# Optimization experiments

Measured on AMD Instinct MI355X. Metric: run time of the kernel, lower is better.

Reference implementation:

```python
import jax, jax.numpy as jnp
from jax import lax
import numpy as np

B, N, D_IN = 8, 8192, 16
GROUP_NUM, K = 512, 32
OUT_DIM, N_BLOCKS, DIM_EXP = 256, 2, 2
PREV_DIM = OUT_DIM // DIM_EXP   # 128
MID = OUT_DIM // 2              # bottleneck width in FeatureTransform
C_EXP = 2 * PREV_DIM + 3        # linear1 input channels
EPS = 1e-5                      # BatchNorm eps (eval mode, running stats mean=0 var=1)


def setup_inputs() -> dict:
    ks = jax.random.split(jax.random.key(0), 8)
    return {
        "xyz": jax.random.normal(ks[0], (B, N, 3), jnp.float32),
        "feat": jax.random.normal(ks[1], (B, N, D_IN), jnp.float32),
        "w_embed": jax.random.normal(ks[2], (PREV_DIM, D_IN), jnp.float32) * 0.1,
        "b_embed": jnp.zeros((PREV_DIM,), jnp.float32),
        "g_embed": jnp.ones((PREV_DIM,), jnp.float32),
        "be_embed": jnp.zeros((PREV_DIM,), jnp.float32),
        "w_lin1": jax.random.normal(ks[3], (OUT_DIM, C_EXP), jnp.float32) * 0.05,
        "g_lin1": jnp.ones((OUT_DIM,), jnp.float32),
        "be_lin1": jnp.zeros((OUT_DIM,), jnp.float32),
        "down_w": jax.random.normal(ks[4], (N_BLOCKS, MID, OUT_DIM), jnp.float32) * 0.05,
        "down_b": jnp.zeros((N_BLOCKS, MID), jnp.float32),
        "gd": jnp.ones((N_BLOCKS, MID), jnp.float32),
        "bd": jnp.zeros((N_BLOCKS, MID), jnp.float32),
        "up_w": jax.random.normal(ks[5], (N_BLOCKS, OUT_DIM, MID), jnp.float32) * 0.05,
        "up_b": jnp.zeros((N_BLOCKS, OUT_DIM), jnp.float32),
        "gu": jnp.ones((N_BLOCKS, OUT_DIM), jnp.float32),
        "bu": jnp.zeros((N_BLOCKS, OUT_DIM), jnp.float32),
    }


def _bn(x, g, b, axis):
    # eval-mode BatchNorm with running mean=0, var=1
    shp = [1] * x.ndim
    shp[axis] = -1
    return x / jnp.sqrt(1.0 + EPS) * g.reshape(shp) + b.reshape(shp)


def _fps(xyz, n):
    # deterministic FPS (eval mode): start from point farthest from origin
    Bb, Nn, _ = xyz.shape
    cur0 = jnp.argmax(jnp.sum(xyz * xyz, -1), axis=1)          # [B]
    mind0 = jnp.full((Bb, Nn), 1e10, xyz.dtype)

    def step(carry, _):
        cur, mind = carry
        c = jnp.take_along_axis(xyz, cur[:, None, None], axis=1)  # [B,1,3]
        mind = jnp.minimum(mind, jnp.sum((xyz - c) ** 2, -1))
        return (jnp.argmax(mind, axis=1), mind), cur

    _, sel = lax.scan(step, (cur0, mind0), None, length=n)     # sel: [n,B]
    return sel.T                                               # [B,n]


def _gather(points, idx):
    # points [B,N,C], idx [B,...] -> [B,...,C]
    Bb = points.shape[0]
    flat = idx.reshape(Bb, -1)
    out = jnp.take_along_axis(points, flat[:, :, None], axis=1)
    return out.reshape(idx.shape + (points.shape[-1],))


def _knn(k, ref, query):
    # squared dists, clamped at 0 as in pairwise_sq_dist
    d = (jnp.sum(query * query, -1)[:, :, None]
         + jnp.sum(ref * ref, -1)[:, None, :]
         - 2.0 * jnp.einsum('bsc,bnc->bsn', query, ref))
    d = jnp.maximum(d, 0.0)
    _, idx = lax.top_k(-d, k)
    return idx  # [B,S,k]


def reference(xyz, feat, w_embed, b_embed, g_embed, be_embed, w_lin1, g_lin1, be_lin1,
              down_w, down_b, gd, bd, up_w, up_b, gu, bu):
    # PointEmbed: conv1d(1x1) + BN + ReLU on per-point features -> [B,N,PREV_DIM]
    f0 = jnp.einsum('bnc,dc->bnd', feat, w_embed) + b_embed
    f0 = jax.nn.relu(_bn(f0, g_embed, be_embed, axis=2))

    # FpsKnnGroup
    sel = _fps(xyz, GROUP_NUM)                  # [B,G]
    lc_xyz = _gather(xyz, sel)                  # [B,G,3]
    lc_feat = _gather(f0, sel)                  # [B,G,PREV_DIM]
    nn_idx = _knn(K, xyz, lc_xyz)               # [B,G,K]
    knn_xyz = _gather(xyz, nn_idx)              # [B,G,K,3]
    knn_feat = jnp.concatenate([_gather(f0, nn_idx), knn_xyz], axis=-1)  # [B,G,K,PREV+3]

    # LocalGeoAgg, norm_type='mn40'
    anchor = lc_xyz[:, :, None, :]
    rel_raw = knn_xyz - anchor
    std = jnp.std(rel_raw, ddof=1) + 1e-5       # torch .std() is unbiased
    knn_xyz_n = rel_raw / std
    Bc = knn_feat.shape[0]
    expanded = jnp.concatenate(
        [knn_feat, jnp.broadcast_to(lc_feat[:, :, None, :], (Bc, GROUP_NUM, K, PREV_DIM))],
        axis=-1)                                # [B,G,K,C_EXP]
    x = jnp.einsum('bgkc,dc->bdgk', expanded, w_lin1)   # linear1 (no bias)
    x = jax.nn.relu(_bn(x, g_lin1, be_lin1, axis=1))    # [B,OUT_DIM,G,K]

    # GaussianPosEnc: rel = normalized knn_xyz (perm) minus raw lc_xyz center
    rel = knn_xyz_n.transpose(0, 3, 1, 2) - lc_xyz.transpose(0, 2, 1)[:, :, :, None]
    w = jnp.exp(-jnp.linalg.norm(rel, axis=1) / 2.0)    # sigma=1 -> 2*sigma^2=2
    x = x * w[:, None, :, :]

    # FeatureTransform residual bottlenecks
    for i in range(N_BLOCKS):
        h = jnp.einsum('bcgk,mc->bmgk', x, down_w[i]) + down_b[i][None, :, None, None]
        h = jax.nn.relu(_bn(h, gd[i], bd[i], axis=1))
        h = jnp.einsum('bcgk,mc->bmgk', h, up_w[i]) + up_b[i][None, :, None, None]
        h = _bn(h, gu[i], bu[i], axis=1)
        x = jax.nn.relu(h + x)

    # MaxMeanPool over K
    return jnp.max(x, axis=-1) + jnp.mean(x, axis=-1)   # [B,OUT_DIM,G]
```

## Files before the change

kernel.cpp:

```cpp
#include <hip/hip_runtime.h>

#define B_ 8
#define N_ 8192
#define DIN_ 16
#define G_ 512
#define K_ 32
#define OD_ 256
#define PD_ 128
#define MD_ 128
#define CE_ 259
#define EST 168
#define XST2 264
#define HST 136
#define AL1K 160

typedef __attribute__((ext_vector_type(8))) short short8t;
typedef __attribute__((ext_vector_type(4))) float f32x4;
typedef __attribute__((ext_vector_type(2))) float v2f;
#define MFMA16(a, b, c) __builtin_amdgcn_mfma_f32_16x16x32_bf16((a), (b), (c), 0, 0, 0)

__device__ __forceinline__ ushort bf16_rne(float x) {
    unsigned u = __float_as_uint(x);
    return (ushort)((u + 0x7FFFu + ((u >> 16) & 1u)) >> 16);
}
__device__ __forceinline__ void bf16_split(float x, ushort& h, ushort& l) {
    h = bf16_rne(x);
    float hf = __uint_as_float((unsigned)h << 16);
    l = bf16_rne(x - hf);
}

#define DPP_STEP_MAXF(x, ctrl) { int _t = __builtin_amdgcn_update_dpp(            \
        __float_as_int(x), __float_as_int(x), (ctrl), 0xF, 0xF, false);           \
        (x) = fmaxf((x), __int_as_float(_t)); }
#define DPP_STEP_MINF(x, ctrl) { int _t = __builtin_amdgcn_update_dpp(            \
        __float_as_int(x), __float_as_int(x), (ctrl), 0xF, 0xF, false);           \
        (x) = fminf((x), __int_as_float(_t)); }
#define DPP_STEP_MINU(x, ctrl) { int _t = __builtin_amdgcn_update_dpp(            \
        (int)(x), (int)(x), (ctrl), 0xF, 0xF, false);                             \
        unsigned _u = (unsigned)_t; (x) = ((x) < _u) ? (x) : _u; }

__device__ __forceinline__ float wave_max_f32(float x) {
    DPP_STEP_MAXF(x, 0x121); DPP_STEP_MAXF(x, 0x122);
    DPP_STEP_MAXF(x, 0x124); DPP_STEP_MAXF(x, 0x128);
    DPP_STEP_MAXF(x, 0x142); DPP_STEP_MAXF(x, 0x143);
    return __int_as_float(__builtin_amdgcn_readlane(__float_as_int(x), 63));
}
__device__ __forceinline__ float wave_min_f32(float x) {
    DPP_STEP_MINF(x, 0x121); DPP_STEP_MINF(x, 0x122);
    DPP_STEP_MINF(x, 0x124); DPP_STEP_MINF(x, 0x128);
    DPP_STEP_MINF(x, 0x142); DPP_STEP_MINF(x, 0x143);
    return __int_as_float(__builtin_amdgcn_readlane(__float_as_int(x), 63));
}
__device__ __forceinline__ unsigned wave_min_u32(unsigned x) {
    DPP_STEP_MINU(x, 0x121); DPP_STEP_MINU(x, 0x122);
    DPP_STEP_MINU(x, 0x124); DPP_STEP_MINU(x, 0x128);
    DPP_STEP_MINU(x, 0x142); DPP_STEP_MINU(x, 0x143);
    return (unsigned)__builtin_amdgcn_readlane((int)x, 63);
}

__global__ __launch_bounds__(256)
void prep_kernel(const float* __restrict__ w_lin1, const float* __restrict__ down_w,
                 const float* __restrict__ up_w, const float* __restrict__ w_embed,
                 float* __restrict__ wta, float* __restrict__ wEtg,
                 ushort* __restrict__ alf, ushort* __restrict__ adf,
                 ushort* __restrict__ auf) {
    int i = blockIdx.x * blockDim.x + threadIdx.x;
    if (i < PD_ * OD_) {
        int j = i >> 8, c = i & 255;
        wta[i] = w_lin1[c * CE_ + 131 + j];
    }
    if (i < DIN_ * PD_) {
        int r = i >> 7, c = i & 127;
        wEtg[i] = w_embed[c * DIN_ + r];
    }
    if (i < 5120) {
        int lane = i & 63, t = i >> 6;
        int kbi = t % 5, mtile = t / 5;
        int m = mtile * 16 + (lane & 15), g16 = lane >> 4;
        int dst = i * 8;
#pragma unroll
        for (int j = 0; j < 8; ++j) {
            int k = kbi * 32 + g16 * 8 + j;
            float v = (k < 131) ? w_lin1[m * CE_ + k] : 0.f;
            ushort h, l; bf16_split(v, h, l);
            alf[dst + j] = h; alf[dst + j + 40960] = l;
        }
    }
    if (i < 8192) {
        int lane = i & 63, t = i >> 6;
        int kbi = t & 7, mtile = (t >> 3) & 7, l = t >> 6;
        int m = mtile * 16 + (lane & 15), g16 = lane >> 4;
        int dst = i * 8;
#pragma unroll
        for (int j = 0; j < 8; ++j) {
            int k = kbi * 32 + g16 * 8 + j;
            float v = down_w[(l * MD_ + m) * OD_ + k];
            ushort h, lo; bf16_split(v, h, lo);
            adf[dst + j] = h; adf[dst + j + 65536] = lo;
        }
    }
    if (i < 8192) {
        int lane = i & 63, t = i >> 6;
        int kbi = t & 3, mtile = (t >> 2) & 15, l = t >> 6;
        int m = mtile * 16 + (lane & 15), g16 = lane >> 4;
        int dst = i * 8;
#pragma unroll
        for (int j = 0; j < 8; ++j) {
            int k = kbi * 32 + g16 * 8 + j;
            float v = up_w[(l * OD_ + m) * MD_ + k];
            ushort h, lo; bf16_split(v, h, lo);
            auf[dst + j] = h; auf[dst + j + 65536] = lo;
        }
    }
}

__global__ __launch_bounds__(512)
void fps_kernel(const float* __restrict__ xyz, int* __restrict__ sel) {
#pragma clang fp contract(off)
    __shared__ float sx[N_], sy[N_], sz[N_];
    __shared__ unsigned long long wred[2][8];
    __shared__ int sel_s[G_];
    int b = blockIdx.x, tid = threadIdx.x;
    const float* xb = xyz + (size_t)b * N_ * 3;
    for (int i = tid; i < N_; i += 512) {
        sx[i] = xb[i * 3]; sy[i] = xb[i * 3 + 1]; sz[i] = xb[i * 3 + 2];
    }
    __syncthreads();
    v2f px2[8], py2[8], pz2[8], mind2[8];
    float bv = -1.f; int bj = 0;
#pragma unroll
    for (int p = 0; p < 8; ++p) {
        int i0 = tid + (2 * p) * 512, i1 = tid + (2 * p + 1) * 512;
        px2[p] = (v2f){sx[i0], sx[i1]};
        py2[p] = (v2f){sy[i0], sy[i1]};
        pz2[p] = (v2f){sz[i0], sz[i1]};
        mind2[p] = (v2f){1e10f, 1e10f};
        v2f ss = px2[p] * px2[p] + py2[p] * py2[p];
        ss = ss + pz2[p] * pz2[p];
        if (ss[0] > bv) { bv = ss[0]; bj = 2 * p; }
        if (ss[1] > bv) { bv = ss[1]; bj = 2 * p + 1; }
    }
    int bi = tid + bj * 512;
    int wv = tid >> 6;
    {
        float wm = wave_max_f32(bv);
        unsigned mi = (bv == wm) ? (unsigned)bi : 0xFFFFFFFFu;
        unsigned wi = wave_min_u32(mi);
        if ((tid & 63) == 0)
            wred[0][wv] = ((unsigned long long)__float_as_uint(wm) << 32)
                        | (unsigned long long)(0xFFFFFFFFu - wi);
    }
    __syncthreads();
    unsigned long long best = wred[0][0];
#pragma unroll
    for (int i = 1; i < 8; ++i) { unsigned long long v = wred[0][i]; if (v > best) best = v; }
    int cur = (int)(0xFFFFFFFFu - (unsigned)(best & 0xFFFFFFFFull));

    for (int it = 0; it < G_; ++it) {
        if (tid == 0) sel_s[it] = cur;
        float cx = sx[cur], cy = sy[cur], cz = sz[cur];
        v2f cx2 = (v2f){cx, cx}, cy2 = (v2f){cy, cy}, cz2 = (v2f){cz, cz};
#pragma unroll
        for (int p = 0; p < 8; ++p) {
            v2f dx = px2[p] - cx2, dy = py2[p] - cy2, dz = pz2[p] - cz2;
            v2f d = dx * dx + dy * dy;
            d = d + dz * dz;
            mind2[p] = __builtin_elementwise_min(mind2[p], d);
        }
        bv = -1.f; bj = 0;
#pragma unroll
        for (int j = 0; j < 16; ++j) {
            float m = mind2[j >> 1][j & 1];
            if (m > bv) { bv = m; bj = j; }
        }
        bi = tid + bj * 512;
        float wm = wave_max_f32(bv);
        unsigned mi = (bv == wm) ? (unsigned)bi : 0xFFFFFFFFu;
        unsigned wi = wave_min_u32(mi);
        int pb = (it + 1) & 1;
        if ((tid & 63) == 0)
            wred[pb][wv] = ((unsigned long long)__float_as_uint(wm) << 32)
                         | (unsigned long long)(0xFFFFFFFFu - wi);
        __syncthreads();
        best = wred[pb][0];
#pragma unroll
        for (int i = 1; i < 8; ++i) { unsigned long long v = wred[pb][i]; if (v > best) best = v; }
        cur = (int)(0xFFFFFFFFu - (unsigned)(best & 0xFFFFFFFFull));
    }
    __syncthreads();
    sel[b * G_ + tid] = sel_s[tid];
}

__global__ __launch_bounds__(256)
void knn_kernel(const float* __restrict__ xyz, const int* __restrict__ sel,
                int* __restrict__ nn) {
#pragma clang fp contract(off)
    __shared__ float dld[N_];
    __shared__ unsigned long long wred[2][4];
    __shared__ int nn_s[K_];
    int gb = blockIdx.x; int b = gb >> 9, s = gb & (G_ - 1);
    const float* xb = xyz + (size_t)b * N_ * 3;
    int q = sel[b * G_ + s];
    float qx = xb[q * 3], qy = xb[q * 3 + 1], qz = xb[q * 3 + 2];
    float qq = (qx * qx + qy * qy) + qz * qz;
    int tid = threadIdx.x;
    const float FINF = __builtin_inff();
    float lv = FINF; int li = tid;
#pragma unroll 4
    for (int j = 0; j < 32; ++j) {
        int n = tid + j * 256;
        float rx = xb[n * 3], ry = xb[n * 3 + 1], rz = xb[n * 3 + 2];
        float rr = (rx * rx + ry * ry) + rz * rz;
        float dt = (qx * rx + qy * ry) + qz * rz;
        float d = (qq + rr) - 2.0f * dt;
        d = fmaxf(d, 0.f);
        dld[n] = d;
        if (d < lv) { lv = d; li = n; }
    }
    {
        float wm = wave_min_f32(lv);
        unsigned mi = (lv == wm) ? (unsigned)li : 0xFFFFFFFFu;
        unsigned wi = wave_min_u32(mi);
        if ((tid & 63) == 0)
            wred[0][tid >> 6] = ((unsigned long long)__float_as_uint(wm) << 32)
                              | (unsigned long long)wi;
    }
    __syncthreads();
    unsigned long long best = wred[0][0];
#pragma unroll
    for (int i = 1; i < 4; ++i) { unsigned long long v = wred[0][i]; if (v < best) best = v; }
    int win = (int)(best & 0xFFFFFFFFull);

    for (int t = 0; t < K_; ++t) {
        if (tid == 0) nn_s[t] = win;
        if ((win & 255) == tid) {
            dld[win] = FINF;
            lv = FINF; li = tid;
            for (int j = 0; j < 32; ++j) {
                float d = dld[tid + j * 256];
                if (d < lv) { lv = d; li = tid + j * 256; }
            }
        }
        float wm = wave_min_f32(lv);
        unsigned mi = (lv == wm) ? (unsigned)li : 0xFFFFFFFFu;
        unsigned wi = wave_min_u32(mi);
        int pb = (t + 1) & 1;
        if ((tid & 63) == 0)
            wred[pb][tid >> 6] = ((unsigned long long)__float_as_uint(wm) << 32)
                               | (unsigned long long)wi;
        __syncthreads();
        best = wred[pb][0];
#pragma unroll
        for (int i = 1; i < 4; ++i) { unsigned long long v = wred[pb][i]; if (v < best) best = v; }
        win = (int)(best & 0xFFFFFFFFull);
    }
    if (tid < K_) nn[(size_t)gb * K_ + tid] = nn_s[tid];
}

__global__ void std_acc_kernel(const float* __restrict__ xyz, const int* __restrict__ sel,
                               const int* __restrict__ nn, double* __restrict__ acc) {
    int tot = B_ * G_ * K_;
    int stride = gridDim.x * blockDim.x;
    double ls = 0.0, lss = 0.0;
    for (int idx = blockIdx.x * blockDim.x + threadIdx.x; idx < tot; idx += stride) {
        int b = idx >> 14; int g = (idx >> 5) & (G_ - 1);
        int n = nn[idx]; int a = sel[b * G_ + g];
        const float* xb = xyz + (size_t)b * N_ * 3;
#pragma unroll
        for (int c = 0; c < 3; ++c) {
            float v = xb[n * 3 + c] - xb[a * 3 + c];
            ls += (double)v; lss += (double)v * (double)v;
        }
    }
#pragma unroll
    for (int off = 32; off > 0; off >>= 1) {
        ls += __shfl_down(ls, off); lss += __shfl_down(lss, off);
    }
    if ((threadIdx.x & 63) == 0) { atomicAdd(acc, ls); atomicAdd(acc + 1, lss); }
}

__global__ void std_fin_kernel(const double* __restrict__ acc, float* __restrict__ stdp) {
    double s = acc[0], ss = acc[1];
    double M = (double)(B_ * G_ * K_ * 3);
    double var = (ss - s * s / M) / (M - 1.0);
    stdp[0] = (float)sqrt(var) + 1e-5f;
}

__global__ __launch_bounds__(256, 3)
void group_kernel(const float* __restrict__ xyz, const float* __restrict__ feat,
                  const float* __restrict__ wEtg, const float* __restrict__ bE,
                  const float* __restrict__ gE, const float* __restrict__ beE,
                  const int* __restrict__ sel, const int* __restrict__ nn,
                  const float* __restrict__ wta,
                  const ushort* __restrict__ alf, const ushort* __restrict__ adf,
                  const ushort* __restrict__ auf,
                  const float* __restrict__ g_lin1, const float* __restrict__ be_lin1,
                  const float* __restrict__ down_b, const float* __restrict__ gd,
                  const float* __restrict__ bd,
                  const float* __restrict__ up_b, const float* __restrict__ gu,
                  const float* __restrict__ bu,
                  const float* __restrict__ stdp, float* __restrict__ out) {
    __shared__ __align__(16) ushort smem[25600];
    __shared__ float lcv_s[OD_];
    __shared__ float wk_s[K_];
    __shared__ int nns_s[K_];
    __shared__ float anch[3];
    ushort* XTh = smem;
    ushort* XTl = smem + 8448;
    ushort* HTh = smem + 16896;
    ushort* HTl = smem + 21248;
    ushort* Ehi = XTh;
    ushort* Elo = XTl;
    float* wEt = (float*)(smem + 16896);
    float* fL  = wEt + 2048;
    float* lcf = fL + 544;

    int gb = blockIdx.x; int b = gb >> 9, g = gb & (G_ - 1);
    int tid = threadIdx.x;
    const float* xb = xyz + (size_t)b * N_ * 3;
    int a = sel[b * G_ + g];
    if (tid < K_) nns_s[tid] = nn[(size_t)gb * K_ + tid];
    if (tid < 3)  anch[tid] = xb[a * 3 + tid];
    __syncthreads();

    for (int idx = tid; idx < DIN_ * PD_; idx += 256) wEt[idx] = wEtg[idx];
    const float* fb = feat + (size_t)b * N_ * DIN_;
    for (int idx = tid; idx < 33 * DIN_; idx += 256) {
        int k = idx >> 4, j = idx & 15;
        int n = (k < K_) ? nns_s[k] : a;
        fL[idx] = fb[(size_t)n * DIN_ + j];
    }
    __syncthreads();

    const float s_bn = 1.0f / sqrtf(1.0f + 1e-5f);
    for (int t = tid; t < 33 * 32; t += 256) {
        int k = t >> 5, c0 = (t & 31) * 4;
        const float* f = &fL[k * DIN_];
        float a0 = 0.f, a1 = 0.f, a2 = 0.f, a3 = 0.f;
#pragma unroll
        for (int i = 0; i < DIN_; ++i) {
            float4 w4 = *(const float4*)&wEt[i * PD_ + c0];
            float fv = f[i];
            a0 += w4.x * fv; a1 += w4.y * fv; a2 += w4.z * fv; a3 += w4.w * fv;
        }
        float4 b4  = *(const float4*)&bE[c0];
        float4 g4  = *(const float4*)&gE[c0];
        float4 be4 = *(const float4*)&beE[c0];
        float o0 = fmaxf((a0 + b4.x) * s_bn * g4.x + be4.x, 0.f);
        float o1 = fmaxf((a1 + b4.y) * s_bn * g4.y + be4.y, 0.f);
        float o2 = fmaxf((a2 + b4.z) * s_bn * g4.z + be4.z, 0.f);
        float o3 = fmaxf((a3 + b4.w) * s_bn * g4.w + be4.w, 0.f);
        if (k < K_) {
            ushort h0, l0, h1, l1, h2, l2, h3, l3;
            bf16_split(o0, h0, l0); bf16_split(o1, h1, l1);
            bf16_split(o2, h2, l2); bf16_split(o3, h3, l3);
            *(ushort4*)&Ehi[k * EST + c0] = make_ushort4(h0, h1, h2, h3);
            *(ushort4*)&Elo[k * EST + c0] = make_ushort4(l0, l1, l2, l3);
        } else {
            *(float4*)&lcf[c0] = make_float4(o0, o1, o2, o3);
        }
    }
    for (int idx = tid; idx < K_ * 32; idx += 256) {
        int k = idx >> 5, c = 128 + (idx & 31);
        ushort h = 0, l = 0;
        if (c < 131) { float v = xb[nns_s[k] * 3 + (c - 128)]; bf16_split(v, h, l); }
        Ehi[k * EST + c] = h; Elo[k * EST + c] = l;
    }
    if (tid < K_) {
#pragma clang fp contract(off)
        float sd = stdp[0];
        int n = nns_s[tid];
        float rx = (xb[n * 3]     - anch[0]) / sd - anch[0];
        float ry = (xb[n * 3 + 1] - anch[1]) / sd - anch[1];
        float rz = (xb[n * 3 + 2] - anch[2]) / sd - anch[2];
        float nrm = sqrtf((rx * rx + ry * ry) + rz * rz);
        wk_s[tid] = expf(-0.5f * nrm);
    }
    __syncthreads();
    {
        float s = 0.f;
        for (int j = 0; j < PD_; ++j) s += wta[j * OD_ + tid] * lcf[j];
        lcv_s[tid] = s;
    }
    __syncthreads();

    int wv = tid >> 6, lane = tid & 63;
    int g16 = lane >> 4, r16 = lane & 15;
    int lane8 = lane * 8;

    f32x4 accl[4][2];
#pragma unroll
    for (int mt = 0; mt < 4; ++mt) {
        int mc = 64 * wv + 16 * mt + 4 * g16;
        float4 lv = *(const float4*)&lcv_s[mc];
        f32x4 iv = {lv.x, lv.y, lv.z, lv.w};
        accl[mt][0] = iv; accl[mt][1] = iv;
    }
    {
        int eb0 = r16 * EST + g16 * 8;
        int eb1 = (r16 + 16) * EST + g16 * 8;
        for (int kbi = 0; kbi < 5; ++kbi) {
            int kb = kbi * 32;
            short8t eh0 = *(const short8t*)&Ehi[eb0 + kb];
            short8t el0 = *(const short8t*)&Elo[eb0 + kb];
            short8t eh1 = *(const short8t*)&Ehi[eb1 + kb];
            short8t el1 = *(const short8t*)&Elo[eb1 + kb];
#pragma unroll
            for (int mt = 0; mt < 4; ++mt) {
                const ushort* wp = alf + (((4 * wv + mt) * 5 + kbi) << 9) + lane8;
                short8t wh = *(const short8t*)wp;
                short8t wl = *(const short8t*)(wp + 40960);
                accl[mt][0] = MFMA16(wh, eh0, accl[mt][0]);
                accl[mt][1] = MFMA16(wh, eh1, accl[mt][1]);
                accl[mt][0] = MFMA16(wh, el0, accl[mt][0]);
                accl[mt][1] = MFMA16(wh, el1, accl[mt][1]);
                accl[mt][0] = MFMA16(wl, eh0, accl[mt][0]);
                accl[mt][1] = MFMA16(wl, eh1, accl[mt][1]);
            }
        }
    }
    __syncthreads();
    {
        float w0 = wk_s[r16], w1 = wk_s[r16 + 16];
#pragma unroll
        for (int mt = 0; mt < 4; ++mt) {
            int mc = 64 * wv + 16 * mt + 4 * g16;
            float4 gg = *(const float4*)&g_lin1[mc];
            float4 bb = *(const float4*)&be_lin1[mc];
            float ga[4] = {gg.x, gg.y, gg.z, gg.w};
            float ba[4] = {bb.x, bb.y, bb.z, bb.w};
            ushort h0[4], l0[4], h1[4], l1[4];
#pragma unroll
            for (int r = 0; r < 4; ++r) {
                float v0 = fmaxf(accl[mt][0][r] * s_bn * ga[r] + ba[r], 0.f) * w0;
                float v1 = fmaxf(accl[mt][1][r] * s_bn * ga[r] + ba[r], 0.f) * w1;
                bf16_split(v0, h0[r], l0[r]);
                bf16_split(v1, h1[r], l1[r]);
            }
            *(ushort4*)&XTh[r16 * XST2 + mc] = make_ushort4(h0[0], h0[1], h0[2], h0[3]);
            *(ushort4*)&XTl[r16 * XST2 + mc] = make_ushort4(l0[0], l0[1], l0[2], l0[3]);
            *(ushort4*)&XTh[(r16 + 16) * XST2 + mc] = make_ushort4(h1[0], h1[1], h1[2], h1[3]);
            *(ushort4*)&XTl[(r16 + 16) * XST2 + mc] = make_ushort4(l1[0], l1[1], l1[2], l1[3]);
        }
    }
    __syncthreads();

    int xbo0 = r16 * XST2 + g16 * 8;
    int xbo1 = (r16 + 16) * XST2 + g16 * 8;
    int hbo0 = r16 * HST + g16 * 8;
    int hbo1 = (r16 + 16) * HST + g16 * 8;
    const f32x4 zz = {0.f, 0.f, 0.f, 0.f};
    const float inv_k = 1.0f / 32.0f;

    for (int l = 0; l < 2; ++l) {
        f32x4 accd[2][2];
        accd[0][0] = zz; accd[0][1] = zz; accd[1][0] = zz; accd[1][1] = zz;
        for (int kbi = 0; kbi < 8; ++kbi) {
            int kb = kbi * 32;
            short8t xh0 = *(const short8t*)&XTh[xbo0 + kb];
            short8t xl0 = *(const short8t*)&XTl[xbo0 + kb];
            short8t xh1 = *(const short8t*)&XTh[xbo1 + kb];
            short8t xl1 = *(const short8t*)&XTl[xbo1 + kb];
#pragma unroll
            for (int mt = 0; mt < 2; ++mt) {
                const ushort* wp = adf + (((l * 8 + (2 * wv + mt)) * 8 + kbi) << 9) + lane8;
                short8t wh = *(const short8t*)wp;
                short8t wl = *(const short8t*)(wp + 65536);
                accd[mt][0] = MFMA16(wh, xh0, accd[mt][0]);
                accd[mt][1] = MFMA16(wh, xh1, accd[mt][1]);
                accd[mt][0] = MFMA16(wh, xl0, accd[mt][0]);
                accd[mt][1] = MFMA16(wh, xl1, accd[mt][1]);
                accd[mt][0] = MFMA16(wl, xh0, accd[mt][0]);
                accd[mt][1] = MFMA16(wl, xh1, accd[mt][1]);
            }
        }
#pragma unroll
        for (int mt = 0; mt < 2; ++mt) {
            int mc = 32 * wv + 16 * mt + 4 * g16;
            float4 db = *(const float4*)&down_b[l * MD_ + mc];
            float4 gv = *(const float4*)&gd[l * MD_ + mc];
            float4 bv = *(const float4*)&bd[l * MD_ + mc];
            float dba[4] = {db.x, db.y, db.z, db.w};
            float gva[4] = {gv.x, gv.y, gv.z, gv.w};
            float bva[4] = {bv.x, bv.y, bv.z, bv.w};
            ushort h0[4], l0[4], h1[4], l1[4];
#pragma unroll
            for (int r = 0; r < 4; ++r) {
                float v0 = fmaxf((accd[mt][0][r] + dba[r]) * s_bn * gva[r] + bva[r], 0.f);
                float v1 = fmaxf((accd[mt][1][r] + dba[r]) * s_bn * gva[r] + bva[r], 0.f);
                bf16_split(v0, h0[r], l0[r]);
                bf16_split(v1, h1[r], l1[r]);
            }
            *(ushort4*)&HTh[r16 * HST + mc] = make_ushort4(h0[0], h0[1], h0[2], h0[3]);
            *(ushort4*)&HTl[r16 * HST + mc] = make_ushort4(l0[0], l0[1], l0[2], l0[3]);
            *(ushort4*)&HTh[(r16 + 16) * HST + mc] = make_ushort4(h1[0], h1[1], h1[2], h1[3]);
            *(ushort4*)&HTl[(r16 + 16) * HST + mc] = make_ushort4(l1[0], l1[1], l1[2], l1[3]);
        }
        __syncthreads();

        f32x4 accu[4][2];
#pragma unroll
        for (int mt = 0; mt < 4; ++mt) { accu[mt][0] = zz; accu[mt][1] = zz; }
        for (int kbi = 0; kbi < 4; ++kbi) {
            int kb = kbi * 32;
            short8t hh0 = *(const short8t*)&HTh[hbo0 + kb];
            short8t hl0 = *(const short8t*)&HTl[hbo0 + kb];
            short8t hh1 = *(const short8t*)&HTh[hbo1 + kb];
            short8t hl1 = *(const short8t*)&HTl[hbo1 + kb];
#pragma unroll
            for (int mt = 0; mt < 4; ++mt) {
                const ushort* wp = auf + (((l * 16 + (4 * wv + mt)) * 4 + kbi) << 9) + lane8;
                short8t wh = *(const short8t*)wp;
                short8t wl = *(const short8t*)(wp + 65536);
                accu[mt][0] = MFMA16(wh, hh0, accu[mt][0]);
                accu[mt][1] = MFMA16(wh, hh1, accu[mt][1]);
                accu[mt][0] = MFMA16(wh, hl0, accu[mt][0]);
                accu[mt][1] = MFMA16(wh, hl1, accu[mt][1]);
                accu[mt][0] = MFMA16(wl, hh0, accu[mt][0]);
                accu[mt][1] = MFMA16(wl, hh1, accu[mt][1]);
            }
        }
#pragma unroll
        for (int mt = 0; mt < 4; ++mt) {
            int mc = 64 * wv + 16 * mt + 4 * g16;
            float4 ub = *(const float4*)&up_b[l * OD_ + mc];
            float4 gv = *(const float4*)&gu[l * OD_ + mc];
            float4 bv = *(const float4*)&bu[l * OD_ + mc];
            float uba[4] = {ub.x, ub.y, ub.z, ub.w};
            float gva[4] = {gv.x, gv.y, gv.z, gv.w};
            float bva[4] = {bv.x, bv.y, bv.z, bv.w};
            ushort4 xh0 = *(const ushort4*)&XTh[r16 * XST2 + mc];
            ushort4 xl0 = *(const ushort4*)&XTl[r16 * XST2 + mc];
            ushort4 xh1 = *(const ushort4*)&XTh[(r16 + 16) * XST2 + mc];
            ushort4 xl1 = *(const ushort4*)&XTl[(r16 + 16) * XST2 + mc];
            ushort xha0[4] = {xh0.x, xh0.y, xh0.z, xh0.w};
            ushort xla0[4] = {xl0.x, xl0.y, xl0.z, xl0.w};
            ushort xha1[4] = {xh1.x, xh1.y, xh1.z, xh1.w};
            ushort xla1[4] = {xl1.x, xl1.y, xl1.z, xl1.w};
            float nx0[4], nx1[4];
#pragma unroll
            for (int r = 0; r < 4; ++r) {
                float xf0 = __uint_as_float((unsigned)xha0[r] << 16) + __uint_as_float((unsigned)xla0[r] << 16);
                float xf1 = __uint_as_float((unsigned)xha1[r] << 16) + __uint_as_float((unsigned)xla1[r] << 16);
                float v0 = (accu[mt][0][r] + uba[r]) * s_bn * gva[r] + bva[r];
                float v1 = (accu[mt][1][r] + uba[r]) * s_bn * gva[r] + bva[r];
                nx0[r] = fmaxf(v0 + xf0, 0.f);
                nx1[r] = fmaxf(v1 + xf1, 0.f);
            }
            if (l == 0) {
                ushort h0[4], l0[4], h1[4], l1[4];
#pragma unroll
                for (int r = 0; r < 4; ++r) {
                    bf16_split(nx0[r], h0[r], l0[r]);
                    bf16_split(nx1[r], h1[r], l1[r]);
                }
                *(ushort4*)&XTh[r16 * XST2 + mc] = make_ushort4(h0[0], h0[1], h0[2], h0[3]);
                *(ushort4*)&XTl[r16 * XST2 + mc] = make_ushort4(l0[0], l0[1], l0[2], l0[3]);
                *(ushort4*)&XTh[(r16 + 16) * XST2 + mc] = make_ushort4(h1[0], h1[1], h1[2], h1[3]);
                *(ushort4*)&XTl[(r16 + 16) * XST2 + mc] = make_ushort4(l1[0], l1[1], l1[2], l1[3]);
            } else {
#pragma unroll
                for (int r = 0; r < 4; ++r) {
                    float mx = fmaxf(nx0[r], nx1[r]);
                    float sm = nx0[r] + nx1[r];
#pragma unroll
                    for (int off = 1; off < 16; off <<= 1) {
                        mx = fmaxf(mx, __shfl_xor(mx, off));
                        sm += __shfl_xor(sm, off);
                    }
                    if (r16 == 0)
                        out[((size_t)(b * OD_ + mc + r)) * G_ + g] = mx + sm * inv_k;
                }
            }
        }
        __syncthreads();
    }
}

extern "C" void kernel_launch(void* const* d_in, const int* in_sizes, int n_in,
                              void* d_out, int out_size, void* d_ws, size_t ws_size,
                              hipStream_t stream) {
    const float* xyz     = (const float*)d_in[0];
    const float* feat    = (const float*)d_in[1];
    const float* w_embed = (const float*)d_in[2];
    const float* b_embed = (const float*)d_in[3];
    const float* g_embed = (const float*)d_in[4];
    const float* be_embed= (const float*)d_in[5];
    const float* w_lin1  = (const float*)d_in[6];
    const float* g_lin1  = (const float*)d_in[7];
    const float* be_lin1 = (const float*)d_in[8];
    const float* down_w  = (const float*)d_in[9];
    const float* down_b  = (const float*)d_in[10];
    const float* gd      = (const float*)d_in[11];
    const float* bd      = (const float*)d_in[12];
    const float* up_w    = (const float*)d_in[13];
    const float* up_b    = (const float*)d_in[14];
    const float* gu      = (const float*)d_in[15];
    const float* bu      = (const float*)d_in[16];
    float* out = (float*)d_out;

    char* w = (char*)d_ws;
    float* wta   = (float*)w;  w += PD_ * OD_ * 4;
    float* wEtg  = (float*)w;  w += DIN_ * PD_ * 4;
    ushort* alf  = (ushort*)w; w += 2 * 40960 * 2;
    ushort* adf  = (ushort*)w; w += 2 * 65536 * 2;
    ushort* auf  = (ushort*)w; w += 2 * 65536 * 2;
    int* sel     = (int*)w;    w += B_ * G_ * 4;
    int* nn      = (int*)w;    w += B_ * G_ * K_ * 4;
    double* acc  = (double*)w; w += 16;
    float* stdp  = (float*)w;

    hipMemsetAsync(acc, 0, 2 * sizeof(double), stream);
    prep_kernel<<<256, 256, 0, stream>>>(w_lin1, down_w, up_w, w_embed,
                                         wta, wEtg, alf, adf, auf);
    fps_kernel<<<B_, 512, 0, stream>>>(xyz, sel);
    knn_kernel<<<B_ * G_, 256, 0, stream>>>(xyz, sel, nn);
    std_acc_kernel<<<256, 256, 0, stream>>>(xyz, sel, nn, acc);
    std_fin_kernel<<<1, 1, 0, stream>>>(acc, stdp);
    group_kernel<<<B_ * G_, 256, 0, stream>>>(xyz, feat, wEtg, b_embed, g_embed, be_embed,
        sel, nn, wta, alf, adf, auf, g_lin1, be_lin1, down_b, gd, bd, up_b, gu, bu, stdp, out);
}
```

Measured before the change: 947.9 us.

## Keep KNN distances in registers, tree-reduce FPS argmax, trim std atomics

The KNN kernel now keeps each thread's 32 distances in a fully unrolled register array instead of a 32 KB shared-memory buffer. This removes LDS traffic and should raise occupancy, at the cost of more VGPRs and a predicated write to clear the winner. The FPS argmax becomes a vector max tree plus an equality mask with ctz, which shortens the serial compare chain. The std reduction now combines waves in shared memory before issuing atomics and launches fewer blocks, and the lcv dot product in group_kernel splits into four accumulators for more ILP, which slightly changes float summation order.

```diff
diff --git a/kernel.cpp b/kernel.cpp
--- a/kernel.cpp
+++ b/kernel.cpp
@@ -167,13 +167,21 @@
             d = d + dz * dz;
             mind2[p] = __builtin_elementwise_min(mind2[p], d);
         }
-        bv = -1.f; bj = 0;
-#pragma unroll
-        for (int j = 0; j < 16; ++j) {
-            float m = mind2[j >> 1][j & 1];
-            if (m > bv) { bv = m; bj = j; }
-        }
+        v2f t0 = __builtin_elementwise_max(mind2[0], mind2[1]);
+        v2f t1 = __builtin_elementwise_max(mind2[2], mind2[3]);
+        v2f t2 = __builtin_elementwise_max(mind2[4], mind2[5]);
+        v2f t3 = __builtin_elementwise_max(mind2[6], mind2[7]);
+        t0 = __builtin_elementwise_max(t0, t1);
+        t2 = __builtin_elementwise_max(t2, t3);
+        t0 = __builtin_elementwise_max(t0, t2);
+        bv = fmaxf(t0[0], t0[1]);
+        unsigned msk = 0;
+#pragma unroll
+        for (int j = 0; j < 16; ++j)
+            if (mind2[j >> 1][j & 1] == bv) msk |= (1u << j);
+        bj = (int)__builtin_ctz(msk);
         bi = tid + bj * 512;
+
         float wm = wave_max_f32(bv);
         unsigned mi = (bv == wm) ? (unsigned)bi : 0xFFFFFFFFu;
         unsigned wi = wave_min_u32(mi);
@@ -195,7 +203,6 @@
 void knn_kernel(const float* __restrict__ xyz, const int* __restrict__ sel,
                 int* __restrict__ nn) {
 #pragma clang fp contract(off)
-    __shared__ float dld[N_];
     __shared__ unsigned long long wred[2][4];
     __shared__ int nn_s[K_];
     int gb = blockIdx.x; int b = gb >> 9, s = gb & (G_ - 1);
@@ -205,8 +212,9 @@
     float qq = (qx * qx + qy * qy) + qz * qz;
     int tid = threadIdx.x;
     const float FINF = __builtin_inff();
+    float dreg[32];
     float lv = FINF; int li = tid;
-#pragma unroll 4
+#pragma unroll
     for (int j = 0; j < 32; ++j) {
         int n = tid + j * 256;
         float rx = xb[n * 3], ry = xb[n * 3 + 1], rz = xb[n * 3 + 2];
@@ -214,7 +222,7 @@
         float dt = (qx * rx + qy * ry) + qz * rz;
         float d = (qq + rr) - 2.0f * dt;
         d = fmaxf(d, 0.f);
-        dld[n] = d;
+        dreg[j] = d;
         if (d < lv) { lv = d; li = n; }
     }
     {
@@ -234,10 +242,13 @@
     for (int t = 0; t < K_; ++t) {
         if (tid == 0) nn_s[t] = win;
         if ((win & 255) == tid) {
-            dld[win] = FINF;
+            int wj = win >> 8;
+#pragma unroll
+            for (int j = 0; j < 32; ++j) if (j == wj) dreg[j] = FINF;
             lv = FINF; li = tid;
+#pragma unroll
             for (int j = 0; j < 32; ++j) {
-                float d = dld[tid + j * 256];
+                float d = dreg[j];
                 if (d < lv) { lv = d; li = tid + j * 256; }
             }
         }
@@ -257,8 +268,10 @@
     if (tid < K_) nn[(size_t)gb * K_ + tid] = nn_s[tid];
 }
 
-__global__ void std_acc_kernel(const float* __restrict__ xyz, const int* __restrict__ sel,
-                               const int* __restrict__ nn, double* __restrict__ acc) {
+__global__ __launch_bounds__(256)
+void std_acc_kernel(const float* __restrict__ xyz, const int* __restrict__ sel,
+                    const int* __restrict__ nn, double* __restrict__ acc) {
+    __shared__ double red[8];
     int tot = B_ * G_ * K_;
     int stride = gridDim.x * blockDim.x;
     double ls = 0.0, lss = 0.0;
@@ -276,7 +289,14 @@
     for (int off = 32; off > 0; off >>= 1) {
         ls += __shfl_down(ls, off); lss += __shfl_down(lss, off);
     }
-    if ((threadIdx.x & 63) == 0) { atomicAdd(acc, ls); atomicAdd(acc + 1, lss); }
+    int wv = threadIdx.x >> 6;
+    if ((threadIdx.x & 63) == 0) { red[wv * 2] = ls; red[wv * 2 + 1] = lss; }
+    __syncthreads();
+    if (threadIdx.x == 0) {
+        double s = (red[0] + red[2]) + (red[4] + red[6]);
+        double ss = (red[1] + red[3]) + (red[5] + red[7]);
+        atomicAdd(acc, s); atomicAdd(acc + 1, ss);
+    }
 }
 
 __global__ void std_fin_kernel(const double* __restrict__ acc, float* __restrict__ stdp) {
@@ -378,9 +398,14 @@
     }
     __syncthreads();
     {
-        float s = 0.f;
-        for (int j = 0; j < PD_; ++j) s += wta[j * OD_ + tid] * lcf[j];
-        lcv_s[tid] = s;
+        float s0 = 0.f, s1 = 0.f, s2 = 0.f, s3 = 0.f;
+        for (int j = 0; j < PD_; j += 4) {
+            s0 += wta[(j    ) * OD_ + tid] * lcf[j    ];
+            s1 += wta[(j + 1) * OD_ + tid] * lcf[j + 1];
+            s2 += wta[(j + 2) * OD_ + tid] * lcf[j + 2];
+            s3 += wta[(j + 3) * OD_ + tid] * lcf[j + 3];
+        }
+        lcv_s[tid] = (s0 + s1) + (s2 + s3);
     }
     __syncthreads();
 
@@ -615,7 +640,7 @@
                                          wta, wEtg, alf, adf, auf);
     fps_kernel<<<B_, 512, 0, stream>>>(xyz, sel);
     knn_kernel<<<B_ * G_, 256, 0, stream>>>(xyz, sel, nn);
-    std_acc_kernel<<<256, 256, 0, stream>>>(xyz, sel, nn, acc);
+    std_acc_kernel<<<64, 256, 0, stream>>>(xyz, sel, nn, acc);
     std_fin_kernel<<<1, 1, 0, stream>>>(acc, stdp);
     group_kernel<<<B_ * G_, 256, 0, stream>>>(xyz, feat, wEtg, b_embed, g_embed, be_embed,
         sel, nn, wta, alf, adf, auf, g_lin1, be_lin1, down_b, gd, bd, up_b, gu, bu, stdp, out);
```

New measurement: 948.5 us. Within noise of the previous version (+0.1%).
